# Kernel tuning notes

Measured on AMD Instinct MI355X. Metric: run time of the kernel, lower is better.

Reference implementation:

```python
import jax, jax.numpy as jnp
import numpy as np

BETA = 0.2


def setup_inputs() -> dict:
    key = jax.random.key(0)
    k1, k2 = jax.random.split(key)
    B, C, H, W = 32, 64, 64, 64  # C == H == W required by the original reshape/permute
    K, D = 512, 64               # num_embeddings, embedding_dim (D == C)
    quant_input = jax.random.normal(k1, (B, C, H, W), dtype=jnp.float32)
    codebook = jax.random.normal(k2, (K, D), dtype=jnp.float32)
    return {"quant_input": quant_input, "codebook": codebook}


def reference(quant_input, codebook):
    B, C, H, W = quant_input.shape
    # (B,C,H,W) -> (B,HW,C)
    x = jnp.transpose(quant_input, (0, 2, 3, 1)).reshape(B, H * W, C)
    # squared euclidean distances (argmin identical to cdist argmin)
    x_sq = jnp.sum(x * x, axis=-1, keepdims=True)          # (B,HW,1)
    e_sq = jnp.sum(codebook * codebook, axis=-1)            # (K,)
    dist = x_sq - 2.0 * jnp.einsum('bnd,kd->bnk', x, codebook) + e_sq  # (B,HW,K)
    encoding_indices = jnp.argmin(dist, axis=-1)            # (B,HW)
    # gather codes, then the original (buggy-but-faithful) reshape/permute
    quant_out = codebook[encoding_indices.reshape(-1)]      # (B*HW, D)
    quant_out = quant_out.reshape(quant_input.shape)        # (B,C,H,W) layout
    quant_out = jnp.transpose(quant_out, (0, 3, 1, 2))      # (B,W,C,H)
    commitment_loss = jnp.mean((jax.lax.stop_gradient(quant_out) - quant_input) ** 2)
    codebook_loss = jnp.mean((quant_out - jax.lax.stop_gradient(quant_input)) ** 2)
    loss = codebook_loss + BETA * commitment_loss
    # straight-through estimator
    quant_out = quant_input + jax.lax.stop_gradient(quant_out - quant_input)
    encoding_indices = encoding_indices.reshape(-1, quant_out.shape[-2], quant_out.shape[-1])
    return quant_out, loss, encoding_indices
```

## Files before the change

kernel.cpp:

```cpp
#include <hip/hip_runtime.h>
#include <math.h>

#define K_CODES 512
#define DIM 64
#define NPTS (32 * 4096)
#define NQ (NPTS * DIM)
#define BPTS 128
#define TAU 2.0e-3f
#define LSCALE (1.2f / 8388608.0f)

typedef _Float16 f16x8 __attribute__((ext_vector_type(8)));
typedef float f32x4 __attribute__((ext_vector_type(4)));


__global__ __launch_bounds__(64) void prep_kernel(const float* __restrict__ cb,
                                                  _Float16* __restrict__ blob,
                                                  float* __restrict__ shalfg,
                                                  float* __restrict__ loss) {
    int k = blockIdx.x, d = threadIdx.x;
    if (k == 0 && d == 0) loss[0] = 0.0f;
    float e = cb[k * DIM + d];
    _Float16 hi = (_Float16)e;
    _Float16 lo = (_Float16)(e - (float)hi);
    int cf = k >> 4, col = k & 15;
    int q = d >> 5, dd = d & 31, kg = dd >> 3, j = dd & 7;
    size_t base = ((size_t)(cf * 4 + q) * 64 + (kg * 16 + col)) * 8 + j;
    blob[base] = hi;
    blob[base + 2 * 64 * 8] = lo;
    float s = e * e;
#pragma unroll
    for (int m = 32; m; m >>= 1) s += __shfl_xor(s, m);
    if (d == 0) shalfg[k] = 0.5f * s;
}

__global__ __launch_bounds__(256, 1) void vq_fused(const float* __restrict__ qin,
                                                   const float* __restrict__ cb,
                                                   const _Float16* __restrict__ blob,
                                                   const float* __restrict__ shalfg,
                                                   float* __restrict__ out,
                                                   float* __restrict__ loss_acc,
                                                   float* __restrict__ idx_out) {
    __shared__ float shs[K_CODES];
    __shared__ int sfinal[BPTS];
    __shared__ float wsum[4];

    const int tid = threadIdx.x, lane = tid & 63, w = tid >> 6;
    const int row16 = lane & 15, kg = lane >> 4;
    const int wp = w * 32;
    const int n0 = blockIdx.x * BPTS;
    const int b = n0 >> 12, hw0 = n0 & 4095;
    const float* qbase = qin + ((size_t)b << 18) + hw0;
    const f16x8* blp = (const f16x8*)blob + lane;

    shs[tid] = shalfg[tid];
    shs[tid + 256] = shalfg[tid + 256];

    f16x8 ah0[2], ah1[2], al0[2], al1[2];
#pragma unroll
    for (int rr = 0; rr < 2; ++rr) {
        const float* xb = qbase + (wp + rr * 16 + row16);
#pragma unroll
        for (int j = 0; j < 8; ++j) {
            float xa = xb[(size_t)(kg * 8 + j) << 12];
            float xc = xb[(size_t)(32 + kg * 8 + j) << 12];
            _Float16 ha = (_Float16)xa, hc = (_Float16)xc;
            ah0[rr][j] = ha; al0[rr][j] = (_Float16)(xa - (float)ha);
            ah1[rr][j] = hc; al1[rr][j] = (_Float16)(xc - (float)hc);
        }
    }
    __syncthreads();

    float b1[8], b2[8];
    int k1[8];
#pragma unroll
    for (int sl = 0; sl < 8; ++sl) { b1[sl] = -INFINITY; b2[sl] = -INFINITY; k1[sl] = 0; }

#define LOADB(P0, P1, P2, P3, CF)              \
    {                                          \
        P0 = blp[((CF) * 4 + 0) * 64];         \
        P1 = blp[((CF) * 4 + 1) * 64];         \
        P2 = blp[((CF) * 4 + 2) * 64];         \
        P3 = blp[((CF) * 4 + 3) * 64];         \
    }
#define CONSUME(CF, B0, B1, BL0, BL1)                                              \
    {                                                                              \
        float sh = shs[(CF) * 16 + row16];                                         \
        f32x4 acA0 = {-sh, -sh, -sh, -sh}, acB0 = {0.f, 0.f, 0.f, 0.f};            \
        f32x4 acA1 = acA0, acB1 = acB0;                                            \
        acA0 = __builtin_amdgcn_mfma_f32_16x16x32_f16(ah0[0], B0, acA0, 0, 0, 0);  \
        acB0 = __builtin_amdgcn_mfma_f32_16x16x32_f16(al0[0], B0, acB0, 0, 0, 0);  \
        acA1 = __builtin_amdgcn_mfma_f32_16x16x32_f16(ah0[1], B0, acA1, 0, 0, 0);  \
        acB1 = __builtin_amdgcn_mfma_f32_16x16x32_f16(al0[1], B0, acB1, 0, 0, 0);  \
        acA0 = __builtin_amdgcn_mfma_f32_16x16x32_f16(ah1[0], B1, acA0, 0, 0, 0);  \
        acB0 = __builtin_amdgcn_mfma_f32_16x16x32_f16(al1[0], B1, acB0, 0, 0, 0);  \
        acA1 = __builtin_amdgcn_mfma_f32_16x16x32_f16(ah1[1], B1, acA1, 0, 0, 0);  \
        acB1 = __builtin_amdgcn_mfma_f32_16x16x32_f16(al1[1], B1, acB1, 0, 0, 0);  \
        acA0 = __builtin_amdgcn_mfma_f32_16x16x32_f16(ah0[0], BL0, acA0, 0, 0, 0); \
        acB0 = __builtin_amdgcn_mfma_f32_16x16x32_f16(ah1[0], BL1, acB0, 0, 0, 0); \
        acA1 = __builtin_amdgcn_mfma_f32_16x16x32_f16(ah0[1], BL0, acA1, 0, 0, 0); \
        acB1 = __builtin_amdgcn_mfma_f32_16x16x32_f16(ah1[1], BL1, acB1, 0, 0, 0); \
        const int kglob = (CF) * 16 + row16;                                       \
        _Pragma("unroll") for (int r = 0; r < 4; ++r) {                            \
            float s_ = acA0[r] + acB0[r];                                          \
            float o1 = b1[r];                                                      \
            bool c1 = s_ > o1;                                                     \
            b2[r] = __builtin_amdgcn_fmed3f(s_, o1, b2[r]);                        \
            b1[r] = c1 ? s_ : o1;                                                  \
            k1[r] = c1 ? kglob : k1[r];                                            \
        }                                                                          \
        _Pragma("unroll") for (int r = 0; r < 4; ++r) {                            \
            float s_ = acA1[r] + acB1[r];                                          \
            float o1 = b1[4 + r];                                                  \
            bool c1 = s_ > o1;                                                     \
            b2[4 + r] = __builtin_amdgcn_fmed3f(s_, o1, b2[4 + r]);                \
            b1[4 + r] = c1 ? s_ : o1;                                              \
            k1[4 + r] = c1 ? kglob : k1[4 + r];                                    \
        }                                                                          \
    }

    f16x8 pa0, pa1, pa2, pa3, qa0, qa1, qa2, qa3;
    LOADB(pa0, pa1, pa2, pa3, 0)
#pragma unroll 1
    for (int cf = 0; cf < 32; cf += 2) {
        LOADB(qa0, qa1, qa2, qa3, cf + 1)
        CONSUME(cf, pa0, pa1, pa2, pa3)
        if (cf + 2 < 32) LOADB(pa0, pa1, pa2, pa3, cf + 2)
        CONSUME(cf + 1, qa0, qa1, qa2, qa3)
    }
#undef LOADB
#undef CONSUME

#pragma unroll
    for (int m = 1; m <= 8; m <<= 1) {
#pragma unroll
        for (int sl = 0; sl < 8; ++sl) {
            float ob1 = __shfl_xor(b1[sl], m);
            float ob2 = __shfl_xor(b2[sl], m);
            int ok1 = __shfl_xor(k1[sl], m);
            float nb2 = fmaxf(fminf(b1[sl], ob1), fmaxf(b2[sl], ob2));
            bool take = (ob1 > b1[sl]) || (ob1 == b1[sl] && ok1 < k1[sl]);
            b1[sl] = take ? ob1 : b1[sl];
            k1[sl] = take ? ok1 : k1[sl];
            b2[sl] = nb2;
        }
    }

    if (row16 == 0) {
#pragma unroll
        for (int sl = 0; sl < 8; ++sl) {
            int pt = wp + (sl >> 2) * 16 + kg * 4 + (sl & 3);
            sfinal[pt] = k1[sl];
            bool fl = (b1[sl] - b2[sl]) < TAU;
            idx_out[n0 + pt] = fl ? -(float)(k1[sl] + 1) : (float)k1[sl];
        }
    }
    __syncthreads();

    {
        int p = tid & 127, hh = tid >> 7;
        int ci = sfinal[p];
        const float* crow = cb + (size_t)ci * DIM + hh * 32;
        const float* qrow = qbase + p + ((size_t)(hh * 32) << 12);
        float* orow = out + ((size_t)b << 18) + hw0 + p + ((size_t)(hh * 32) << 12);
        float l0 = 0.f, l1 = 0.f, l2 = 0.f, l3 = 0.f;
#pragma unroll
        for (int d = 0; d < 32; d += 4) {
            float4 v = *(const float4*)(crow + d);
            orow[(size_t)(d + 0) << 12] = v.x;
            orow[(size_t)(d + 1) << 12] = v.y;
            orow[(size_t)(d + 2) << 12] = v.z;
            orow[(size_t)(d + 3) << 12] = v.w;
            float q0 = qrow[(size_t)(d + 0) << 12];
            float q1 = qrow[(size_t)(d + 1) << 12];
            float q2 = qrow[(size_t)(d + 2) << 12];
            float q3 = qrow[(size_t)(d + 3) << 12];
            float e0 = v.x - q0, e1 = v.y - q1, e2 = v.z - q2, e3 = v.w - q3;
            l0 = fmaf(e0, e0, l0); l1 = fmaf(e1, e1, l1);
            l2 = fmaf(e2, e2, l2); l3 = fmaf(e3, e3, l3);
        }
        float s = (l0 + l1) + (l2 + l3);
#pragma unroll
        for (int off = 32; off > 0; off >>= 1) s += __shfl_down(s, off);
        if (lane == 0) wsum[w] = s;
    }
    __syncthreads();
    if (tid == 0)
        atomicAdd(loss_acc, LSCALE * ((wsum[0] + wsum[1]) + (wsum[2] + wsum[3])));
}

__global__ __launch_bounds__(256, 1) void vq_fixup(const float* __restrict__ qin,
                                                   const float* __restrict__ cb,
                                                   const float* __restrict__ shalfg,
                                                   float* __restrict__ idx_out,
                                                   float* __restrict__ out,
                                                   float* __restrict__ loss_acc) {
    const int lane = threadIdx.x & 63;
    const int nb = (blockIdx.x * 4 + (threadIdx.x >> 6)) * 64;
    float v = idx_out[nb + lane];
    unsigned long long mask = __ballot(v < 0.0f);
    while (mask) {
        int src = __ffsll((long long)mask) - 1;
        mask &= mask - 1;
        int n = nb + src;
        int oldk = (int)(-__shfl(v, src)) - 1;
        int b = n >> 12, hw = n & 4095;
        const float* qx = qin + ((size_t)b << 18) + hw;
        float x[DIM];
#pragma unroll
        for (int d = 0; d < DIM; ++d) x[d] = qx[(size_t)d << 12];
        float bs = -INFINITY;
        int bi = 0;
#pragma unroll 1
        for (int i2 = 0; i2 < 8; ++i2) {
            int k = i2 * 64 + lane;
            const float4* c4 = (const float4*)(cb + (size_t)k * DIM);
            float d0 = 0.f, d1 = 0.f, d2 = 0.f, d3 = 0.f;
#pragma unroll
            for (int j = 0; j < 16; ++j) {
                float4 c = c4[j];
                d0 = fmaf(x[4 * j + 0], c.x, d0);
                d1 = fmaf(x[4 * j + 1], c.y, d1);
                d2 = fmaf(x[4 * j + 2], c.z, d2);
                d3 = fmaf(x[4 * j + 3], c.w, d3);
            }
            float sc = ((d0 + d1) + (d2 + d3)) - shalfg[k];
            if (sc > bs) { bs = sc; bi = k; }
        }
#pragma unroll
        for (int m = 1; m < 64; m <<= 1) {
            float os = __shfl_xor(bs, m);
            int oi = __shfl_xor(bi, m);
            if (os > bs || (os == bs && oi < bi)) { bs = os; bi = oi; }
        }
        if (lane == 0) idx_out[n] = (float)bi;
        if (bi != oldk) {
            float xd = x[lane];
            float nv = cb[(size_t)bi * DIM + lane];
            float ov = cb[(size_t)oldk * DIM + lane];
            float en = nv - xd, eo = ov - xd;
            float delta = en * en - eo * eo;
#pragma unroll
            for (int m = 32; m > 0; m >>= 1) delta += __shfl_down(delta, m);
            out[((size_t)b << 18) + ((size_t)lane << 12) + hw] = nv;
            if (lane == 0) atomicAdd(loss_acc, LSCALE * delta);
        }
    }
}

extern "C" void kernel_launch(void* const* d_in, const int* in_sizes, int n_in,
                              void* d_out, int out_size, void* d_ws, size_t ws_size,
                              hipStream_t stream) {
    const float* qin = (const float*)d_in[0];
    const float* cb = (const float*)d_in[1];
    float* out = (float*)d_out;
    float* loss_out = out + NQ;
    float* idx_out = out + NQ + 1;

    _Float16* blob = (_Float16*)d_ws;
    float* shalfg = (float*)((char*)d_ws + 131072);

    prep_kernel<<<K_CODES, 64, 0, stream>>>(cb, blob, shalfg, loss_out);
    vq_fused<<<NPTS / BPTS, 256, 0, stream>>>(qin, cb, blob, shalfg, out, loss_out, idx_out);
    vq_fixup<<<NPTS / 256, 256, 0, stream>>>(qin, cb, shalfg, idx_out, out, loss_out);
}
```

Measured before the change: 72.51 us.

## Split codebook search across two wave groups per block and merge top-2 in LDS

Doubles the fused kernel's block to 512 threads. Each half of the waves scans half of the 512 codes for the same 128 points, and the per-half best, second-best and index are then merged through shared memory. The gather/loss epilogue is spread across all 512 threads. The aim is more waves in flight per CU to hide MFMA and load latency, at the cost of loading and splitting the A fragments twice, plus an extra LDS merge and barrier.

```diff
diff --git a/kernel.cpp b/kernel.cpp
--- a/kernel.cpp
+++ b/kernel.cpp
@@ -33,7 +33,7 @@
     if (d == 0) shalfg[k] = 0.5f * s;
 }
 
-__global__ __launch_bounds__(256, 1) void vq_fused(const float* __restrict__ qin,
+__global__ __launch_bounds__(512, 1) void vq_fused(const float* __restrict__ qin,
                                                    const float* __restrict__ cb,
                                                    const _Float16* __restrict__ blob,
                                                    const float* __restrict__ shalfg,
@@ -41,19 +41,22 @@
                                                    float* __restrict__ loss_acc,
                                                    float* __restrict__ idx_out) {
     __shared__ float shs[K_CODES];
+    __shared__ float sb1[2][BPTS], sb2[2][BPTS];
+    __shared__ int sk1[2][BPTS];
     __shared__ int sfinal[BPTS];
-    __shared__ float wsum[4];
+    __shared__ float wsum[8];
 
     const int tid = threadIdx.x, lane = tid & 63, w = tid >> 6;
+    const int half = w >> 2;
+    const int wq = w & 3;
     const int row16 = lane & 15, kg = lane >> 4;
-    const int wp = w * 32;
+    const int wp = wq * 32;
     const int n0 = blockIdx.x * BPTS;
     const int b = n0 >> 12, hw0 = n0 & 4095;
     const float* qbase = qin + ((size_t)b << 18) + hw0;
     const f16x8* blp = (const f16x8*)blob + lane;
 
     shs[tid] = shalfg[tid];
-    shs[tid + 256] = shalfg[tid + 256];
 
     f16x8 ah0[2], ah1[2], al0[2], al1[2];
 #pragma unroll
@@ -118,14 +121,17 @@
         }                                                                          \
     }
 
-    f16x8 pa0, pa1, pa2, pa3, qa0, qa1, qa2, qa3;
-    LOADB(pa0, pa1, pa2, pa3, 0)
+    {
+        const int cf0 = half * 16;
+        f16x8 pa0, pa1, pa2, pa3, qa0, qa1, qa2, qa3;
+        LOADB(pa0, pa1, pa2, pa3, cf0)
 #pragma unroll 1
-    for (int cf = 0; cf < 32; cf += 2) {
-        LOADB(qa0, qa1, qa2, qa3, cf + 1)
-        CONSUME(cf, pa0, pa1, pa2, pa3)
-        if (cf + 2 < 32) LOADB(pa0, pa1, pa2, pa3, cf + 2)
-        CONSUME(cf + 1, qa0, qa1, qa2, qa3)
+        for (int cf = cf0; cf < cf0 + 16; cf += 2) {
+            LOADB(qa0, qa1, qa2, qa3, cf + 1)
+            CONSUME(cf, pa0, pa1, pa2, pa3)
+            if (cf + 2 < cf0 + 16) LOADB(pa0, pa1, pa2, pa3, cf + 2)
+            CONSUME(cf + 1, qa0, qa1, qa2, qa3)
+        }
     }
 #undef LOADB
 #undef CONSUME
@@ -149,22 +155,36 @@
 #pragma unroll
         for (int sl = 0; sl < 8; ++sl) {
             int pt = wp + (sl >> 2) * 16 + kg * 4 + (sl & 3);
-            sfinal[pt] = k1[sl];
-            bool fl = (b1[sl] - b2[sl]) < TAU;
-            idx_out[n0 + pt] = fl ? -(float)(k1[sl] + 1) : (float)k1[sl];
-        }
+            sb1[half][pt] = b1[sl];
+            sb2[half][pt] = b2[sl];
+            sk1[half][pt] = k1[sl];
+        }
+    }
+    __syncthreads();
+
+    if (tid < BPTS) {
+        float a1 = sb1[0][tid], a2 = sb2[0][tid];
+        float c1 = sb1[1][tid], c2 = sb2[1][tid];
+        int ka = sk1[0][tid], kc = sk1[1][tid];
+        bool takeB = c1 > a1;
+        float t1 = takeB ? c1 : a1;
+        int tk = takeB ? kc : ka;
+        float t2 = fmaxf(fminf(a1, c1), fmaxf(a2, c2));
+        sfinal[tid] = tk;
+        bool fl = (t1 - t2) < TAU;
+        idx_out[n0 + tid] = fl ? -(float)(tk + 1) : (float)tk;
     }
     __syncthreads();
 
     {
         int p = tid & 127, hh = tid >> 7;
         int ci = sfinal[p];
-        const float* crow = cb + (size_t)ci * DIM + hh * 32;
-        const float* qrow = qbase + p + ((size_t)(hh * 32) << 12);
-        float* orow = out + ((size_t)b << 18) + hw0 + p + ((size_t)(hh * 32) << 12);
+        const float* crow = cb + (size_t)ci * DIM + hh * 16;
+        const float* qrow = qbase + p + ((size_t)(hh * 16) << 12);
+        float* orow = out + ((size_t)b << 18) + hw0 + p + ((size_t)(hh * 16) << 12);
         float l0 = 0.f, l1 = 0.f, l2 = 0.f, l3 = 0.f;
 #pragma unroll
-        for (int d = 0; d < 32; d += 4) {
+        for (int d = 0; d < 16; d += 4) {
             float4 v = *(const float4*)(crow + d);
             orow[(size_t)(d + 0) << 12] = v.x;
             orow[(size_t)(d + 1) << 12] = v.y;
@@ -184,8 +204,12 @@
         if (lane == 0) wsum[w] = s;
     }
     __syncthreads();
-    if (tid == 0)
-        atomicAdd(loss_acc, LSCALE * ((wsum[0] + wsum[1]) + (wsum[2] + wsum[3])));
+    if (tid == 0) {
+        float t = 0.f;
+#pragma unroll
+        for (int i = 0; i < 8; ++i) t += wsum[i];
+        atomicAdd(loss_acc, LSCALE * t);
+    }
 }
 
 __global__ __launch_bounds__(256, 1) void vq_fixup(const float* __restrict__ qin,
@@ -260,6 +284,6 @@
     float* shalfg = (float*)((char*)d_ws + 131072);
 
     prep_kernel<<<K_CODES, 64, 0, stream>>>(cb, blob, shalfg, loss_out);
-    vq_fused<<<NPTS / BPTS, 256, 0, stream>>>(qin, cb, blob, shalfg, out, loss_out, idx_out);
+    vq_fused<<<NPTS / BPTS, 512, 0, stream>>>(qin, cb, blob, shalfg, out, loss_out, idx_out);
     vq_fixup<<<NPTS / 256, 256, 0, stream>>>(qin, cb, shalfg, idx_out, out, loss_out);
 }
```

Result: slower. 83.70 us (+15.4%).
